# Kernel optimization log

Hardware: AMD Instinct MI355X
Metric: run time of the kernel (lower is better)

The kernel has to match this reference:

```python
import jax, jax.numpy as jnp
import numpy as np
from functools import partial

GRID = 5  # 224/32 - 2
N_ANCHORS = 3
N_BOX = GRID * GRID * N_ANCHORS  # 75


def _make_anchors():
    # faithful replication of _create_anchors (grid-index cx,cy with pixel-scale w,h)
    scales = [56, 112, 224]
    a = np.zeros((GRID, GRID, N_ANCHORS, 8), np.float32)
    for x in range(GRID):
        for y in range(GRID):
            for k in range(N_ANCHORS):
                w = h = scales[k]
                a[x, y, k] = [x - w // 2, y - h // 2, x + w // 2, y + h // 2, x, y, w, h]
    return jnp.asarray(a)

ANCHORS = _make_anchors()  # [5,5,3,8]: x0,y0,x1,y1,cx,cy,w,h


def conv2d(x, w, b, pad):
    y = jax.lax.conv_general_dilated(x, w, (1, 1), [(pad, pad), (pad, pad)],
                                     dimension_numbers=('NCHW', 'OIHW', 'NCHW'))
    return y + b[None, :, None, None]


def maxpool2(x):
    return jax.lax.reduce_window(x, -jnp.inf, jax.lax.max,
                                 (1, 1, 2, 2), (1, 1, 2, 2), 'VALID')


def deparam_bboxes(rp_reg):
    # rp_reg: [B,5,5,3,4]; anchors broadcast over batch
    aw = ANCHORS[..., 6]; ah = ANCHORS[..., 7]
    ax = ANCHORS[..., 4]; ay = ANCHORS[..., 5]
    cx = rp_reg[..., 0] * aw + ax
    cy = rp_reg[..., 1] * ah + ay
    w = jnp.exp(rp_reg[..., 2]) * aw
    h = jnp.exp(rp_reg[..., 3]) * ah
    return jnp.stack([cx - w / 2, cy - h / 2, cx + w / 2, cy + h / 2], axis=-1)


def _iou_as_written(bi, bj):
    # replicates bb_intersection_over_union EXACTLY, including the missing
    # parentheses bug: inter/areaA + areaB - inter
    xA = jnp.maximum(bi[0], bj[..., 0]); yA = jnp.maximum(bi[1], bj[..., 1])
    xB = jnp.minimum(bi[2], bj[..., 2]); yB = jnp.minimum(bi[3], bj[..., 3])
    inter = jnp.maximum(0.0, xB - xA + 1) * jnp.maximum(0.0, yB - yA + 1)
    areaA = (bi[2] - bi[0] + 1) * (bi[3] - bi[1] + 1)
    areaB = (bj[..., 2] - bj[..., 0] + 1) * (bj[..., 3] - bj[..., 1] + 1)
    return inter / areaA + areaB - inter


def nms_single(boxes, scores, thresh=0.7):
    # boxes [75,4], scores [75]; greedy suppression in score order (vectorized
    # replacement of the O(n^2) Python-loop NMS in _compute_bboxes)
    order = jnp.argsort(-scores)
    b = boxes[order]
    idx = jnp.arange(N_BOX)

    def body(i, keep):
        iou = _iou_as_written(b[i], b)          # [75]
        sup = (idx > i) & (iou > thresh) & keep[i]
        return keep & ~sup

    keep_sorted = jax.lax.fori_loop(0, N_BOX, body, jnp.ones(N_BOX, bool))
    return jnp.zeros(N_BOX, bool).at[order].set(keep_sorted)


def setup_inputs() -> dict:
    key = jax.random.key(0)
    ks = jax.random.split(key, 16)
    B = 32
    inp = {"x": jax.random.normal(ks[0], (B, 3, 224, 224), jnp.float32)}
    chans = [3, 64, 128, 256, 512, 512]
    for i in range(5):
        cin, cout = chans[i], chans[i + 1]
        std = float(np.sqrt(2.0 / (cout * 9)))  # kaiming fan_out, relu
        inp[f"fw{i}"] = jax.random.normal(ks[1 + i], (cout, cin, 3, 3), jnp.float32) * std
        inp[f"fb{i}"] = jnp.zeros((cout,), jnp.float32)
    # RPN heads: normal(0, 0.01), zero bias (per _initialize_rp_weights)
    inp["rpw_w"] = jax.random.normal(ks[6], (512, 512, 3, 3), jnp.float32) * 0.01
    inp["rpw_b"] = jnp.zeros((512,), jnp.float32)
    inp["cls_w"] = jax.random.normal(ks[7], (N_ANCHORS, 512, 1, 1), jnp.float32) * 0.01
    inp["cls_b"] = jnp.zeros((N_ANCHORS,), jnp.float32)
    inp["reg_w"] = jax.random.normal(ks[8], (4 * N_ANCHORS, 512, 1, 1), jnp.float32) * 0.01
    inp["reg_b"] = jnp.zeros((4 * N_ANCHORS,), jnp.float32)
    # classifier2: Linear(512*7*7, 20), normal(0, 0.01)
    inp["fc_w"] = jax.random.normal(ks[9], (20, 512 * 7 * 7), jnp.float32) * 0.01
    inp["fc_b"] = jnp.zeros((20,), jnp.float32)
    return inp


def reference(x, fw0, fb0, fw1, fb1, fw2, fb2, fw3, fb3, fw4, fb4,
              rpw_w, rpw_b, cls_w, cls_b, reg_w, reg_b, fc_w, fc_b):
    B = x.shape[0]
    feat = x
    for w, b in ((fw0, fb0), (fw1, fb1), (fw2, fb2), (fw3, fb3), (fw4, fb4)):
        feat = maxpool2(jax.nn.relu(conv2d(feat, w, b, pad=1)))
    # feat: [B,512,7,7]
    rp512 = jax.nn.relu(conv2d(feat, rpw_w, rpw_b, pad=0))          # [B,512,5,5]
    rp_cls = jax.nn.sigmoid(conv2d(rp512, cls_w, cls_b, pad=0))     # [B,3,5,5]
    rp_reg = conv2d(rp512, reg_w, reg_b, pad=0)                     # [B,12,5,5]
    # faithful to torch .view (row-major reshape, NOT permute)
    rp_cls = rp_cls.reshape(B, GRID, GRID, N_ANCHORS)
    rp_reg = rp_reg.reshape(B, GRID, GRID, N_ANCHORS, 4)
    bboxes = deparam_bboxes(rp_reg)                                 # [B,5,5,3,4]
    keep = jax.vmap(nms_single)(bboxes.reshape(B, N_BOX, 4),
                                rp_cls.reshape(B, N_BOX))           # [B,75] bool
    logits = feat.reshape(B, -1) @ fc_w.T + fc_b                    # [B,20]
    return logits, rp_cls, rp_reg, bboxes, keep
```

## Files before the change

kernel.cpp:

```cpp
#include <hip/hip_runtime.h>
#include <math.h>


#define OFF_LOGITS 0
#define OFF_CLS    640
#define OFF_REG    3040
#define OFF_BOXES  12640
#define OFF_KEEP   22240

constexpr int BATCH = 32;

typedef _Float16 h8 __attribute__((ext_vector_type(8)));
typedef _Float16 h4 __attribute__((ext_vector_type(4)));
typedef float    f4 __attribute__((ext_vector_type(4)));

#define MFMA16(a, b, c) __builtin_amdgcn_mfma_f32_16x16x32_f16(a, b, c, 0, 0, 0)

#if defined(__has_builtin)
#  if __has_builtin(__builtin_amdgcn_global_load_lds)
#    define HAS_GLL 1
#  endif
#endif

__device__ __forceinline__ void stage16(const _Float16* g, _Float16* lbase, int lane) {
#ifdef HAS_GLL
  __builtin_amdgcn_global_load_lds((const __attribute__((address_space(1))) void*)g,
                                   (__attribute__((address_space(3))) void*)lbase,
                                   16, 0, 0);
#else
  *reinterpret_cast<h8*>(lbase + lane * 8) = *reinterpret_cast<const h8*>(g);
#endif
}

constexpr size_t A_OFF = 0;
constexpr size_t B_OFF = 106463232;
constexpr size_t W_OFF = 161579008;
constexpr size_t P_OFF = A_OFF + 8388608;

constexpr int I0_E = 26615808;
constexpr int I1_E = 13778944;
constexpr int I2_E = 7372800;
constexpr int I3_E = 4194304;
constexpr int I4_E = 802816;

__global__ __launch_bounds__(256)
void wcvt(const float* __restrict__ src, _Float16* __restrict__ dHi,
          _Float16* __restrict__ dLo, int COUT, int CIN) {
  const int total = COUT * CIN * 9;
  for (int idx = blockIdx.x * 256 + threadIdx.x; idx < total; idx += gridDim.x * 256) {
    const int co = idx / (CIN * 9);
    const int r = idx % (CIN * 9);
    const int ci = r / 9, tap = r % 9;
    const float v = src[idx];
    const _Float16 h = (_Float16)v;
    const int o = ((tap * (CIN >> 5) + (ci >> 5)) * COUT + co) * 32 + (ci & 31);
    dHi[o] = h;
    dLo[o] = (_Float16)(v - (float)h);
  }
}

__global__ __launch_bounds__(256)
void zero_ring(_Float16* __restrict__ hi, _Float16* __restrict__ lo, int P, int C) {
  const int c8n = C / 8, cells = 4 * P - 4;
  const int tot = 32 * cells * c8n;
  for (int idx = blockIdx.x * 256 + threadIdx.x; idx < tot; idx += gridDim.x * 256) {
    const int c8 = idx % c8n;
    const int cell = (idx / c8n) % cells;
    const int n = idx / (c8n * cells);
    int y, xx;
    if (cell < 2 * P) { y = (cell < P) ? 0 : (P - 1); xx = cell % P; }
    else { const int q = cell - 2 * P; y = 1 + (q >> 1); xx = (q & 1) ? (P - 1) : 0; }
    const long o = ((long)(n * P + y) * P + xx) * C + c8 * 8;
    h8 z = {};
    *reinterpret_cast<h8*>(hi + o) = z;
    *reinterpret_cast<h8*>(lo + o) = z;
  }
}

__global__ __launch_bounds__(256)
void conv_l0(const float* __restrict__ x, const float* __restrict__ w0,
             const float* __restrict__ b0, _Float16* __restrict__ outHi,
             _Float16* __restrict__ outLo) {
  const int bid = blockIdx.x;
  const int tx0 = (bid % 7) * 16, ty0 = ((bid / 7) % 7) * 16, n = bid / 49;
  __shared__ float sIn[3 * 34 * 34];
  __shared__ float sW[1728];
  __shared__ float sB[64];
  const int tid = threadIdx.x;
  for (int idx = tid; idx < 3 * 34 * 34; idx += 256) {
    const int ci = idx / 1156, rem = idx % 1156, r = rem / 34, cc = rem % 34;
    const int y = 2 * ty0 - 1 + r, xx = 2 * tx0 - 1 + cc;
    float v = 0.f;
    if ((unsigned)y < 224u && (unsigned)xx < 224u)
      v = x[((n * 3 + ci) * 224 + y) * 224 + xx];
    sIn[idx] = v;
  }
  for (int idx = tid; idx < 1728; idx += 256) sW[idx] = w0[idx];
  if (tid < 64) sB[tid] = b0[tid];
  __syncthreads();

  const int tpy = tid / 16, tpx = tid % 16;
  float win[3][4][4];
  #pragma unroll
  for (int ci = 0; ci < 3; ++ci)
    #pragma unroll
    for (int dr = 0; dr < 4; ++dr)
      #pragma unroll
      for (int dc = 0; dc < 4; ++dc)
        win[ci][dr][dc] = sIn[ci * 1156 + (2 * tpy + dr) * 34 + (2 * tpx + dc)];

  const long ob = ((long)(n * 114 + ty0 + tpy + 1) * 114 + tx0 + tpx + 1) * 64;
  for (int co4 = 0; co4 < 16; ++co4) {
    h4 hh, ll;
    #pragma unroll
    for (int j = 0; j < 4; ++j) {
      const int co = co4 * 4 + j;
      float a00 = 0.f, a01 = 0.f, a10 = 0.f, a11 = 0.f;
      #pragma unroll
      for (int ci = 0; ci < 3; ++ci)
        #pragma unroll
        for (int ky = 0; ky < 3; ++ky)
          #pragma unroll
          for (int kx = 0; kx < 3; ++kx) {
            const float wv = sW[co * 27 + ci * 9 + ky * 3 + kx];
            a00 = fmaf(win[ci][ky][kx], wv, a00);
            a01 = fmaf(win[ci][ky][kx + 1], wv, a01);
            a10 = fmaf(win[ci][ky + 1][kx], wv, a10);
            a11 = fmaf(win[ci][ky + 1][kx + 1], wv, a11);
          }
      const float p = fmaxf(fmaxf(fmaxf(a00, a01), fmaxf(a10, a11)) + sB[co], 0.f);
      const _Float16 h = (_Float16)p;
      hh[j] = h;
      ll[j] = (_Float16)(p - (float)h);
    }
    *reinterpret_cast<h4*>(outHi + ob + co4 * 4) = hh;
    *reinterpret_cast<h4*>(outLo + ob + co4 * 4) = ll;
  }
}

template<int CIN, int COUT, int H, int BCO, int BSP, int TG, int MODE>
__global__ __launch_bounds__(256)
void convpool(const _Float16* __restrict__ inHi, const _Float16* __restrict__ inLo,
              const _Float16* __restrict__ wHi, const _Float16* __restrict__ wLo,
              const float* __restrict__ bias, _Float16* __restrict__ outHi,
              _Float16* __restrict__ outLo, float* __restrict__ outF) {
  constexpr int W = H, Hp = H / 2, Wp = W / 2, PW = W + 2, POW = Wp + 2;
  constexpr int NCOW = BCO / 64, NSPW = BSP / 64;
  static_assert(NCOW * NSPW == 4, "4 waves");
  constexpr int KCH = CIN / 32;
  constexpr int NCH = TG * KCH;
  constexpr int NISS = BSP / 64;
  constexpr int SPTOT = 32 * H * W;
  __align__(16) __shared__ _Float16 sB[2][2][BSP * 32];

  const int tid = threadIdx.x;
  const int lane = tid & 63, wv = tid >> 6;
  const int c = lane & 15, kq = lane >> 4;
  const int cow = blockIdx.y * BCO + (wv % NCOW) * 64;
  const int spl = (wv / NCOW) * 64;
  const int sblk = blockIdx.x * BSP;
  const int tap0 = (TG == 9) ? 0 : blockIdx.z * TG;

  int gstage[NISS];
  #pragma unroll
  for (int i = 0; i < NISS; ++i) {
    const int sl = i * 64 + tid / 4;
    const int sg = sblk + sl;
    const int ry = sg & 1, tt = sg >> 1;
    const int x = tt % W, u = tt / W;
    const int py = u % Hp, n = u / Hp;
    gstage[i] = ((n * (H + 2) + 2 * py + ry) * PW + x) * CIN + (((tid & 3) ^ (sl & 3)) * 8);
  }
  int dsoff[4];
  #pragma unroll
  for (int nt = 0; nt < 4; ++nt) {
    const int row = spl + nt * 16 + c;
    dsoff[nt] = row * 32 + ((kq ^ (c & 3)) * 8);
  }

  {
    const int tb = ((tap0 / 3) * PW + (tap0 % 3)) * CIN;
    #pragma unroll
    for (int i = 0; i < NISS; ++i) {
      stage16(inHi + gstage[i] + tb, &sB[0][0][i * 2048 + wv * 512], lane);
      stage16(inLo + gstage[i] + tb, &sB[0][1][i * 2048 + wv * 512], lane);
    }
  }
  __syncthreads();

  f4 acc[4][4] = {};
  int cur = 0;
  for (int ch = 0; ch < NCH; ++ch) {
    const int tap = tap0 + ch / KCH;
    const int kcI = ch % KCH;
    h8 aH[4], aL[4];
    const long abase = ((long)(tap * KCH + kcI) * COUT + cow) * 32;
    #pragma unroll
    for (int mt = 0; mt < 4; ++mt) {
      const long ao = abase + (mt * 16 + c) * 32 + kq * 8;
      aH[mt] = *reinterpret_cast<const h8*>(wHi + ao);
      aL[mt] = *reinterpret_cast<const h8*>(wLo + ao);
    }
    if (ch + 1 < NCH) {
      const int tap2 = tap0 + (ch + 1) / KCH;
      const int tb2 = ((tap2 / 3) * PW + (tap2 % 3)) * CIN + ((ch + 1) % KCH) * 32;
      #pragma unroll
      for (int i = 0; i < NISS; ++i) {
        stage16(inHi + gstage[i] + tb2, &sB[cur ^ 1][0][i * 2048 + wv * 512], lane);
        stage16(inLo + gstage[i] + tb2, &sB[cur ^ 1][1][i * 2048 + wv * 512], lane);
      }
    }
    h8 bH[4], bL[4];
    #pragma unroll
    for (int nt = 0; nt < 4; ++nt) {
      bH[nt] = *reinterpret_cast<const h8*>(&sB[cur][0][dsoff[nt]]);
      bL[nt] = *reinterpret_cast<const h8*>(&sB[cur][1][dsoff[nt]]);
    }
    #pragma unroll
    for (int mt = 0; mt < 4; ++mt)
      #pragma unroll
      for (int nt = 0; nt < 4; ++nt)
        acc[mt][nt] = MFMA16(aH[mt], bH[nt], acc[mt][nt]);
    #pragma unroll
    for (int mt = 0; mt < 4; ++mt)
      #pragma unroll
      for (int nt = 0; nt < 4; ++nt)
        acc[mt][nt] = MFMA16(aH[mt], bL[nt], acc[mt][nt]);
    #pragma unroll
    for (int mt = 0; mt < 4; ++mt)
      #pragma unroll
      for (int nt = 0; nt < 4; ++nt)
        acc[mt][nt] = MFMA16(aL[mt], bH[nt], acc[mt][nt]);
    __syncthreads();
    cur ^= 1;
  }

  const int r4 = lane >> 4;
  if (MODE == 1) {
    #pragma unroll
    for (int mt = 0; mt < 4; ++mt) {
      const int co0 = cow + mt * 16 + r4 * 4;
      #pragma unroll
      for (int nt = 0; nt < 4; ++nt) {
        const int s = sblk + spl + nt * 16 + c;
        *reinterpret_cast<f4*>(outF + ((long)blockIdx.z * SPTOT + s) * COUT + co0) =
            acc[mt][nt];
      }
    }
  } else {
    #pragma unroll
    for (int mt = 0; mt < 4; ++mt) {
      const int co0 = cow + mt * 16 + r4 * 4;
      const f4 bi = *reinterpret_cast<const f4*>(bias + co0);
      #pragma unroll
      for (int nt = 0; nt < 4; ++nt) {
        f4 v = acc[mt][nt];
        #pragma unroll
        for (int r = 0; r < 4; ++r) {
          const float m1 = fmaxf(v[r], __shfl_xor(v[r], 1, 64));
          v[r] = fmaxf(m1, __shfl_xor(m1, 2, 64));
        }
        if ((lane & 3) == 0) {
          const int s = sblk + spl + nt * 16 + c;
          const int ps = s >> 2;
          const int n = ps / (Hp * Wp), rem = ps % (Hp * Wp);
          const int py = rem / Wp, px = rem % Wp;
          h4 hh, ll;
          #pragma unroll
          for (int r = 0; r < 4; ++r) {
            const float p = fmaxf(v[r] + bi[r], 0.f);
            const _Float16 h = (_Float16)p;
            hh[r] = h;
            ll[r] = (_Float16)(p - (float)h);
          }
          const long oa = ((long)((n * (Hp + 2) + py + 1) * POW + px + 1)) * COUT + co0;
          *reinterpret_cast<h4*>(outHi + oa) = hh;
          *reinterpret_cast<h4*>(outLo + oa) = ll;
        }
      }
    }
  }
}

__global__ __launch_bounds__(256)
void l4_finish(const float* __restrict__ part, const float* __restrict__ bias,
               _Float16* __restrict__ I4h, _Float16* __restrict__ I4l,
               float* __restrict__ feat) {
  const int t = blockIdx.x * 256 + threadIdx.x;
  if (t >= 1568 * 128) return;
  const int co0 = (t % 128) * 4, p = t / 128;
  f4 m;
  #pragma unroll
  for (int q = 0; q < 4; ++q) {
    const long s = 4L * p + q;
    f4 v = *reinterpret_cast<const f4*>(part + s * 512 + co0);
    v += *reinterpret_cast<const f4*>(part + (6272 + s) * 512 + co0);
    v += *reinterpret_cast<const f4*>(part + (12544 + s) * 512 + co0);
    if (q == 0) m = v;
    else {
      #pragma unroll
      for (int r = 0; r < 4; ++r) m[r] = fmaxf(m[r], v[r]);
    }
  }
  const f4 bi = *reinterpret_cast<const f4*>(bias + co0);
  h4 hh, ll;
  const int n = p / 49, pix = p % 49;
  #pragma unroll
  for (int r = 0; r < 4; ++r) {
    const float pv = fmaxf(m[r] + bi[r], 0.f);
    const _Float16 h = (_Float16)pv;
    hh[r] = h;
    ll[r] = (_Float16)(pv - (float)h);
    feat[((long)(n * 512 + co0 + r)) * 49 + pix] = pv;
  }
  *reinterpret_cast<h4*>(I4h + (long)p * 512 + co0) = hh;
  *reinterpret_cast<h4*>(I4l + (long)p * 512 + co0) = ll;
}

__global__ __launch_bounds__(256)
void rpn_partial(const _Float16* __restrict__ inHi, const _Float16* __restrict__ inLo,
                 const _Float16* __restrict__ wHi, const _Float16* __restrict__ wLo,
                 float* __restrict__ part) {
  const int lane = threadIdx.x & 63, wv = threadIdx.x >> 6;
  const int cow = blockIdx.y * 128 + wv * 32;
  const int sblk = blockIdx.x * 64;
  const int tap = blockIdx.z, ky = tap / 3, kx = tap % 3;
  const int c = lane & 15, kq = lane >> 4;

  int baseB[4];
  #pragma unroll
  for (int nt = 0; nt < 4; ++nt) {
    int s = sblk + nt * 16 + c;
    if (s > 799) s = 799;
    const int n = s / 25, pix = s % 25, py = pix / 5, px = pix % 5;
    baseB[nt] = ((n * 7 + py + ky) * 7 + px + kx) * 512;
  }

  f4 acc[2][4] = {};
  for (int kch = 0; kch < 16; ++kch) {
    h8 aH[2], aL[2], bH[4], bL[4];
    const long abase = ((long)(tap * 16 + kch) * 512 + cow) * 32;
    #pragma unroll
    for (int mt = 0; mt < 2; ++mt) {
      const long ao = abase + (mt * 16 + c) * 32 + kq * 8;
      aH[mt] = *reinterpret_cast<const h8*>(wHi + ao);
      aL[mt] = *reinterpret_cast<const h8*>(wLo + ao);
    }
    #pragma unroll
    for (int nt = 0; nt < 4; ++nt) {
      const int bo = baseB[nt] + kch * 32 + kq * 8;
      bH[nt] = *reinterpret_cast<const h8*>(inHi + bo);
      bL[nt] = *reinterpret_cast<const h8*>(inLo + bo);
    }
    #pragma unroll
    for (int mt = 0; mt < 2; ++mt)
      #pragma unroll
      for (int nt = 0; nt < 4; ++nt)
        acc[mt][nt] = MFMA16(aH[mt], bH[nt], acc[mt][nt]);
    #pragma unroll
    for (int mt = 0; mt < 2; ++mt)
      #pragma unroll
      for (int nt = 0; nt < 4; ++nt)
        acc[mt][nt] = MFMA16(aH[mt], bL[nt], acc[mt][nt]);
    #pragma unroll
    for (int mt = 0; mt < 2; ++mt)
      #pragma unroll
      for (int nt = 0; nt < 4; ++nt)
        acc[mt][nt] = MFMA16(aL[mt], bH[nt], acc[mt][nt]);
  }

  const int r4 = lane >> 4;
  #pragma unroll
  for (int mt = 0; mt < 2; ++mt) {
    const int co0 = cow + mt * 16 + r4 * 4;
    #pragma unroll
    for (int nt = 0; nt < 4; ++nt) {
      const int s = sblk + nt * 16 + c;
      if (s < 800)
        *reinterpret_cast<f4*>(part + ((long)tap * 800 + s) * 512 + co0) = acc[mt][nt];
    }
  }
}

__global__ __launch_bounds__(256)
void rpn_finish(const float* __restrict__ part, const float* __restrict__ bias,
                float* __restrict__ rp512) {
  const int t = blockIdx.x * 256 + threadIdx.x;
  if (t >= 800 * 128) return;
  const int co0 = (t % 128) * 4, s = t / 128;
  f4 acc = *reinterpret_cast<const f4*>(bias + co0);
  #pragma unroll
  for (int g = 0; g < 9; ++g)
    acc += *reinterpret_cast<const f4*>(part + ((long)g * 800 + s) * 512 + co0);
  f4 o;
  #pragma unroll
  for (int r = 0; r < 4; ++r) o[r] = fmaxf(acc[r], 0.f);
  *reinterpret_cast<f4*>(rp512 + (long)s * 512 + co0) = o;
}

__global__ __launch_bounds__(256)
void heads_kernel(const float* __restrict__ rp512,
                  const float* __restrict__ cls_w, const float* __restrict__ cls_b,
                  const float* __restrict__ reg_w, const float* __restrict__ reg_b,
                  float* __restrict__ out) {
  const int idx = blockIdx.x * 256 + threadIdx.x;
  if (idx >= 32 * 25 * 15) return;
  const int o = idx % 15, pix = (idx / 15) % 25, n = idx / 375;
  const float* __restrict__ ip = rp512 + ((long)(n * 25 + pix)) * 512;
  const float* __restrict__ wvp = (o < 3) ? (cls_w + o * 512) : (reg_w + (o - 3) * 512);
  float acc = 0.f;
  for (int k = 0; k < 512; k += 4) {
    const f4 a = *reinterpret_cast<const f4*>(ip + k);
    const f4 b = *reinterpret_cast<const f4*>(wvp + k);
    acc = fmaf(a[0], b[0], acc); acc = fmaf(a[1], b[1], acc);
    acc = fmaf(a[2], b[2], acc); acc = fmaf(a[3], b[3], acc);
  }
  if (o < 3) {
    acc += cls_b[o];
    out[OFF_CLS + n * 75 + o * 25 + pix] = 1.f / (1.f + expf(-acc));
  } else {
    acc += reg_b[o - 3];
    out[OFF_REG + n * 300 + (o - 3) * 25 + pix] = acc;
  }
}

__global__ __launch_bounds__(256)
void fc_kernel(const float* __restrict__ feat, const float* __restrict__ fw,
               const float* __restrict__ fb, float* __restrict__ out) {
  const int n = blockIdx.x, j = blockIdx.y;
  const float* __restrict__ ip = feat + (long)n * 25088;
  const float* __restrict__ wj = fw + (long)j * 25088;
  float acc = 0.f;
  for (int k = threadIdx.x * 4; k < 25088; k += 1024) {
    const f4 a = *reinterpret_cast<const f4*>(ip + k);
    const f4 b = *reinterpret_cast<const f4*>(wj + k);
    acc = fmaf(a[0], b[0], acc); acc = fmaf(a[1], b[1], acc);
    acc = fmaf(a[2], b[2], acc); acc = fmaf(a[3], b[3], acc);
  }
  #pragma unroll
  for (int m = 32; m >= 1; m >>= 1) acc += __shfl_xor(acc, m, 64);
  __shared__ float red[4];
  const int wv = threadIdx.x >> 6;
  if ((threadIdx.x & 63) == 0) red[wv] = acc;
  __syncthreads();
  if (threadIdx.x == 0)
    out[OFF_LOGITS + n * 20 + j] = red[0] + red[1] + red[2] + red[3] + fb[j];
}

__global__ __launch_bounds__(128)
void bbox_nms_kernel(float* __restrict__ out) {
  const int n = blockIdx.x;
  const int t = threadIdx.x;
  __shared__ float bx0[75], by0[75], bx1[75], by1[75], area[75], sc[75];
  __shared__ int rank_s[75], order_s[75], keep_s[75];

  if (t < 75) {
    const int g1 = t / 15, g2 = (t / 3) % 5, a = t % 3;
    const float aw = (a == 0) ? 56.f : (a == 1 ? 112.f : 224.f);
    const float r0 = out[OFF_REG + n * 300 + 4 * t + 0];
    const float r1 = out[OFF_REG + n * 300 + 4 * t + 1];
    const float r2 = out[OFF_REG + n * 300 + 4 * t + 2];
    const float r3 = out[OFF_REG + n * 300 + 4 * t + 3];
    const float cx = r0 * aw + (float)g1;
    const float cy = r1 * aw + (float)g2;
    const float w_ = expf(r2) * aw;
    const float h_ = expf(r3) * aw;
    const float x0 = cx - 0.5f * w_, y0 = cy - 0.5f * h_;
    const float x1 = cx + 0.5f * w_, y1 = cy + 0.5f * h_;
    bx0[t] = x0; by0[t] = y0; bx1[t] = x1; by1[t] = y1;
    area[t] = (x1 - x0 + 1.f) * (y1 - y0 + 1.f);
    out[OFF_BOXES + n * 300 + 4 * t + 0] = x0;
    out[OFF_BOXES + n * 300 + 4 * t + 1] = y0;
    out[OFF_BOXES + n * 300 + 4 * t + 2] = x1;
    out[OFF_BOXES + n * 300 + 4 * t + 3] = y1;
    sc[t] = out[OFF_CLS + n * 75 + t];
    keep_s[t] = 1;
  }
  __syncthreads();
  if (t < 75) {
    const float si = sc[t];
    int rk = 0;
    for (int j = 0; j < 75; ++j) {
      const float sj = sc[j];
      rk += (sj > si) || (sj == si && j < t);
    }
    rank_s[t] = rk;
    order_s[rk] = t;
  }
  __syncthreads();
  for (int i = 0; i < 74; ++i) {
    if (keep_s[i]) {
      const int bi = order_s[i];
      if (t > i && t < 75) {
        const int bj = order_s[t];
        const float xA = fmaxf(bx0[bi], bx0[bj]);
        const float yA = fmaxf(by0[bi], by0[bj]);
        const float xB = fminf(bx1[bi], bx1[bj]);
        const float yB = fminf(by1[bi], by1[bj]);
        const float inter = fmaxf(0.f, xB - xA + 1.f) * fmaxf(0.f, yB - yA + 1.f);
        const float iou = inter / area[bi] + area[bj] - inter;
        if (iou > 0.7f) keep_s[t] = 0;
      }
    }
    __syncthreads();
  }
  if (t < 75) out[OFF_KEEP + n * 75 + t] = keep_s[rank_s[t]] ? 1.f : 0.f;
}

extern "C" void kernel_launch(void* const* d_in, const int* in_sizes, int n_in,
                              void* d_out, int out_size, void* d_ws, size_t ws_size,
                              hipStream_t stream) {
  (void)in_sizes; (void)n_in; (void)out_size; (void)ws_size;
  const float* x     = (const float*)d_in[0];
  const float* fw0   = (const float*)d_in[1];
  const float* fb0   = (const float*)d_in[2];
  const float* fw1   = (const float*)d_in[3];
  const float* fb1   = (const float*)d_in[4];
  const float* fw2   = (const float*)d_in[5];
  const float* fb2   = (const float*)d_in[6];
  const float* fw3   = (const float*)d_in[7];
  const float* fb3   = (const float*)d_in[8];
  const float* fw4   = (const float*)d_in[9];
  const float* fb4   = (const float*)d_in[10];
  const float* rpw_w = (const float*)d_in[11];
  const float* rpw_b = (const float*)d_in[12];
  const float* cls_w = (const float*)d_in[13];
  const float* cls_b = (const float*)d_in[14];
  const float* reg_w = (const float*)d_in[15];
  const float* reg_b = (const float*)d_in[16];
  const float* fc_w  = (const float*)d_in[17];
  const float* fc_b  = (const float*)d_in[18];
  float* out = (float*)d_out;
  char* ws = (char*)d_ws;

  _Float16* I0h = (_Float16*)(ws + A_OFF);
  _Float16* I0l = I0h + I0_E;
  _Float16* I1h = (_Float16*)(ws + B_OFF);
  _Float16* I1l = I1h + I1_E;
  _Float16* I2h = (_Float16*)(ws + A_OFF);
  _Float16* I2l = I2h + I2_E;
  _Float16* I3h = (_Float16*)(ws + B_OFF);
  _Float16* I3l = I3h + I3_E;
  _Float16* I4h = (_Float16*)(ws + A_OFF);
  _Float16* I4l = I4h + I4_E;
  float* feat  = (float*)(ws + A_OFF + (size_t)I4_E * 4);
  float* rp512 = (float*)(ws + A_OFF + (size_t)I4_E * 4 + 3211264);
  float* part  = (float*)(ws + P_OFF);

  _Float16* w1h = (_Float16*)(ws + W_OFF);                _Float16* w1l = w1h + 73728;
  _Float16* w2h = (_Float16*)(ws + W_OFF + 294912);       _Float16* w2l = w2h + 294912;
  _Float16* w3h = (_Float16*)(ws + W_OFF + 1474560);      _Float16* w3l = w3h + 1179648;
  _Float16* w4h = (_Float16*)(ws + W_OFF + 6193152);      _Float16* w4l = w4h + 2359296;
  _Float16* wrh = (_Float16*)(ws + W_OFF + 15630336);     _Float16* wrl = wrh + 2359296;

  wcvt<<<(73728 + 255) / 256, 256, 0, stream>>>(fw1, w1h, w1l, 128, 64);
  wcvt<<<(294912 + 255) / 256, 256, 0, stream>>>(fw2, w2h, w2l, 256, 128);
  wcvt<<<(1179648 + 255) / 256, 256, 0, stream>>>(fw3, w3h, w3l, 512, 256);
  wcvt<<<(2359296 + 255) / 256, 256, 0, stream>>>(fw4, w4h, w4l, 512, 512);
  wcvt<<<(2359296 + 255) / 256, 256, 0, stream>>>(rpw_w, wrh, wrl, 512, 512);

  zero_ring<<<512, 256, 0, stream>>>(I0h, I0l, 114, 64);
  zero_ring<<<512, 256, 0, stream>>>(I1h, I1l, 58, 128);

  conv_l0<<<32 * 49, 256, 0, stream>>>(x, fw0, fb0, I0h, I0l);

  convpool<64, 128, 112, 128, 128, 9, 0><<<dim3(3136, 1, 1), 256, 0, stream>>>(
      I0h, I0l, w1h, w1l, fb1, I1h, I1l, nullptr);
  zero_ring<<<512, 256, 0, stream>>>(I2h, I2l, 30, 256);
  convpool<128, 256, 56, 256, 64, 9, 0><<<dim3(1568, 1, 1), 256, 0, stream>>>(
      I1h, I1l, w2h, w2l, fb2, I2h, I2l, nullptr);
  zero_ring<<<512, 256, 0, stream>>>(I3h, I3l, 16, 512);
  convpool<256, 512, 28, 256, 64, 9, 0><<<dim3(392, 2, 1), 256, 0, stream>>>(
      I2h, I2l, w3h, w3l, fb3, I3h, I3l, nullptr);
  convpool<512, 512, 14, 256, 64, 3, 1><<<dim3(98, 2, 3), 256, 0, stream>>>(
      I3h, I3l, w4h, w4l, nullptr, nullptr, nullptr, part);
  l4_finish<<<(1568 * 128 + 255) / 256, 256, 0, stream>>>(part, fb4, I4h, I4l, feat);

  rpn_partial<<<dim3(13, 4, 9), 256, 0, stream>>>(I4h, I4l, wrh, wrl, part);
  rpn_finish<<<(800 * 128 + 255) / 256, 256, 0, stream>>>(part, rpw_b, rp512);

  heads_kernel<<<(12000 + 255) / 256, 256, 0, stream>>>(rp512, cls_w, cls_b, reg_w, reg_b, out);
  fc_kernel<<<dim3(32, 20), 256, 0, stream>>>(feat, fc_w, fc_b, out);
  bbox_nms_kernel<<<BATCH, 128, 0, stream>>>(out);
}
```

Measured before the change: 1.060 ms.

## Stage multiple K-chunks per barrier phase in convpool and change LDS swizzle

The convpool main loop now groups KPH consecutive 32-wide K chunks into one phase. All chunks of the next phase are staged into double-buffered LDS together, and only one __syncthreads runs per phase instead of per chunk. Layers 2–4 use KPH=2, which halves barrier count but doubles LDS footprint and may reduce occupancy. The LDS XOR swizzle also changes to use (row>>1)&3, aiming to reduce bank conflicts on the B-fragment reads.

```diff
diff --git a/kernel.cpp b/kernel.cpp
--- a/kernel.cpp
+++ b/kernel.cpp
@@ -138,7 +138,7 @@
   }
 }
 
-template<int CIN, int COUT, int H, int BCO, int BSP, int TG, int MODE>
+template<int CIN, int COUT, int H, int BCO, int BSP, int TG, int KPH, int MODE>
 __global__ __launch_bounds__(256)
 void convpool(const _Float16* __restrict__ inHi, const _Float16* __restrict__ inLo,
               const _Float16* __restrict__ wHi, const _Float16* __restrict__ wLo,
@@ -149,9 +149,13 @@
   static_assert(NCOW * NSPW == 4, "4 waves");
   constexpr int KCH = CIN / 32;
   constexpr int NCH = TG * KCH;
+  constexpr int NPH = NCH / KPH;
+  static_assert(NCH % KPH == 0, "even phases");
   constexpr int NISS = BSP / 64;
   constexpr int SPTOT = 32 * H * W;
-  __align__(16) __shared__ _Float16 sB[2][2][BSP * 32];
+  constexpr int TSZ = BSP * 32;
+  __align__(16) __shared__ _Float16 sB[2 * 2 * KPH * TSZ];
+  #define TIDX(buf, hl, j) ((((buf) * 2 + (hl)) * KPH + (j)) * TSZ)
 
   const int tid = threadIdx.x;
   const int lane = tid & 63, wv = tid >> 6;
@@ -169,71 +173,85 @@
     const int ry = sg & 1, tt = sg >> 1;
     const int x = tt % W, u = tt / W;
     const int py = u % Hp, n = u / Hp;
-    gstage[i] = ((n * (H + 2) + 2 * py + ry) * PW + x) * CIN + (((tid & 3) ^ (sl & 3)) * 8);
+    gstage[i] = ((n * (H + 2) + 2 * py + ry) * PW + x) * CIN +
+                (((tid & 3) ^ ((sl >> 1) & 3)) * 8);
   }
   int dsoff[4];
   #pragma unroll
   for (int nt = 0; nt < 4; ++nt) {
     const int row = spl + nt * 16 + c;
-    dsoff[nt] = row * 32 + ((kq ^ (c & 3)) * 8);
-  }
-
-  {
-    const int tb = ((tap0 / 3) * PW + (tap0 % 3)) * CIN;
+    dsoff[nt] = row * 32 + ((kq ^ ((row >> 1) & 3)) * 8);
+  }
+
+  #pragma unroll
+  for (int j = 0; j < KPH; ++j) {
+    const int tap = tap0 + j / KCH, kc = j % KCH;
+    const int tb = ((tap / 3) * PW + (tap % 3)) * CIN + kc * 32;
     #pragma unroll
     for (int i = 0; i < NISS; ++i) {
-      stage16(inHi + gstage[i] + tb, &sB[0][0][i * 2048 + wv * 512], lane);
-      stage16(inLo + gstage[i] + tb, &sB[0][1][i * 2048 + wv * 512], lane);
+      stage16(inHi + gstage[i] + tb, &sB[TIDX(0, 0, j) + i * 2048 + wv * 512], lane);
+      stage16(inLo + gstage[i] + tb, &sB[TIDX(0, 1, j) + i * 2048 + wv * 512], lane);
     }
   }
   __syncthreads();
 
   f4 acc[4][4] = {};
   int cur = 0;
-  for (int ch = 0; ch < NCH; ++ch) {
-    const int tap = tap0 + ch / KCH;
-    const int kcI = ch % KCH;
-    h8 aH[4], aL[4];
-    const long abase = ((long)(tap * KCH + kcI) * COUT + cow) * 32;
-    #pragma unroll
-    for (int mt = 0; mt < 4; ++mt) {
-      const long ao = abase + (mt * 16 + c) * 32 + kq * 8;
-      aH[mt] = *reinterpret_cast<const h8*>(wHi + ao);
-      aL[mt] = *reinterpret_cast<const h8*>(wLo + ao);
-    }
-    if (ch + 1 < NCH) {
-      const int tap2 = tap0 + (ch + 1) / KCH;
-      const int tb2 = ((tap2 / 3) * PW + (tap2 % 3)) * CIN + ((ch + 1) % KCH) * 32;
-      #pragma unroll
-      for (int i = 0; i < NISS; ++i) {
-        stage16(inHi + gstage[i] + tb2, &sB[cur ^ 1][0][i * 2048 + wv * 512], lane);
-        stage16(inLo + gstage[i] + tb2, &sB[cur ^ 1][1][i * 2048 + wv * 512], lane);
+  for (int ph = 0; ph < NPH; ++ph) {
+    #pragma unroll
+    for (int j = 0; j < KPH; ++j) {
+      const int ch = ph * KPH + j;
+      const int tap = tap0 + ch / KCH;
+      const int kc = ch % KCH;
+      h8 aH[4], aL[4];
+      const long abase = ((long)(tap * KCH + kc) * COUT + cow) * 32;
+      #pragma unroll
+      for (int mt = 0; mt < 4; ++mt) {
+        const long ao = abase + (mt * 16 + c) * 32 + kq * 8;
+        aH[mt] = *reinterpret_cast<const h8*>(wHi + ao);
+        aL[mt] = *reinterpret_cast<const h8*>(wLo + ao);
       }
-    }
-    h8 bH[4], bL[4];
-    #pragma unroll
-    for (int nt = 0; nt < 4; ++nt) {
-      bH[nt] = *reinterpret_cast<const h8*>(&sB[cur][0][dsoff[nt]]);
-      bL[nt] = *reinterpret_cast<const h8*>(&sB[cur][1][dsoff[nt]]);
-    }
-    #pragma unroll
-    for (int mt = 0; mt < 4; ++mt)
-      #pragma unroll
-      for (int nt = 0; nt < 4; ++nt)
-        acc[mt][nt] = MFMA16(aH[mt], bH[nt], acc[mt][nt]);
-    #pragma unroll
-    for (int mt = 0; mt < 4; ++mt)
-      #pragma unroll
-      for (int nt = 0; nt < 4; ++nt)
-        acc[mt][nt] = MFMA16(aH[mt], bL[nt], acc[mt][nt]);
-    #pragma unroll
-    for (int mt = 0; mt < 4; ++mt)
-      #pragma unroll
-      for (int nt = 0; nt < 4; ++nt)
-        acc[mt][nt] = MFMA16(aL[mt], bH[nt], acc[mt][nt]);
+      if (j == 0 && ph + 1 < NPH) {
+        #pragma unroll
+        for (int j2 = 0; j2 < KPH; ++j2) {
+          const int ch2 = (ph + 1) * KPH + j2;
+          const int tap2 = tap0 + ch2 / KCH;
+          const int tb2 = ((tap2 / 3) * PW + (tap2 % 3)) * CIN + (ch2 % KCH) * 32;
+          #pragma unroll
+          for (int i = 0; i < NISS; ++i) {
+            stage16(inHi + gstage[i] + tb2,
+                    &sB[TIDX(cur ^ 1, 0, j2) + i * 2048 + wv * 512], lane);
+            stage16(inLo + gstage[i] + tb2,
+                    &sB[TIDX(cur ^ 1, 1, j2) + i * 2048 + wv * 512], lane);
+          }
+        }
+      }
+      h8 bH[4], bL[4];
+      #pragma unroll
+      for (int nt = 0; nt < 4; ++nt) {
+        bH[nt] = *reinterpret_cast<const h8*>(&sB[TIDX(cur, 0, j) + dsoff[nt]]);
+        bL[nt] = *reinterpret_cast<const h8*>(&sB[TIDX(cur, 1, j) + dsoff[nt]]);
+      }
+      #pragma unroll
+      for (int mt = 0; mt < 4; ++mt)
+        #pragma unroll
+        for (int nt = 0; nt < 4; ++nt)
+          acc[mt][nt] = MFMA16(aH[mt], bH[nt], acc[mt][nt]);
+      #pragma unroll
+      for (int mt = 0; mt < 4; ++mt)
+        #pragma unroll
+        for (int nt = 0; nt < 4; ++nt)
+          acc[mt][nt] = MFMA16(aH[mt], bL[nt], acc[mt][nt]);
+      #pragma unroll
+      for (int mt = 0; mt < 4; ++mt)
+        #pragma unroll
+        for (int nt = 0; nt < 4; ++nt)
+          acc[mt][nt] = MFMA16(aL[mt], bH[nt], acc[mt][nt]);
+    }
     __syncthreads();
     cur ^= 1;
   }
+  #undef TIDX
 
   const int r4 = lane >> 4;
   if (MODE == 1) {
@@ -564,15 +582,15 @@
 
   conv_l0<<<32 * 49, 256, 0, stream>>>(x, fw0, fb0, I0h, I0l);
 
-  convpool<64, 128, 112, 128, 128, 9, 0><<<dim3(3136, 1, 1), 256, 0, stream>>>(
+  convpool<64, 128, 112, 128, 128, 9, 1, 0><<<dim3(3136, 1, 1), 256, 0, stream>>>(
       I0h, I0l, w1h, w1l, fb1, I1h, I1l, nullptr);
   zero_ring<<<512, 256, 0, stream>>>(I2h, I2l, 30, 256);
-  convpool<128, 256, 56, 256, 64, 9, 0><<<dim3(1568, 1, 1), 256, 0, stream>>>(
+  convpool<128, 256, 56, 256, 64, 9, 2, 0><<<dim3(1568, 1, 1), 256, 0, stream>>>(
       I1h, I1l, w2h, w2l, fb2, I2h, I2l, nullptr);
   zero_ring<<<512, 256, 0, stream>>>(I3h, I3l, 16, 512);
-  convpool<256, 512, 28, 256, 64, 9, 0><<<dim3(392, 2, 1), 256, 0, stream>>>(
+  convpool<256, 512, 28, 256, 64, 9, 2, 0><<<dim3(392, 2, 1), 256, 0, stream>>>(
       I2h, I2l, w3h, w3l, fb3, I3h, I3l, nullptr);
-  convpool<512, 512, 14, 256, 64, 3, 1><<<dim3(98, 2, 3), 256, 0, stream>>>(
+  convpool<512, 512, 14, 256, 64, 3, 2, 1><<<dim3(98, 2, 3), 256, 0, stream>>>(
       I3h, I3l, w4h, w4l, nullptr, nullptr, nullptr, part);
   l4_finish<<<(1568 * 128 + 255) / 256, 256, 0, stream>>>(part, fb4, I4h, I4l, feat);
 
```

New measurement: 1.017 ms. 1.04x faster.
